# Performance work log

Measured on AMD Instinct MI355X. Metric: run time of the kernel, lower is better.

## Reference

```python
import jax, jax.numpy as jnp
import numpy as np

K = 10  # num_s nearest neighbors


def setup_inputs() -> dict:
    key = jax.random.key(0)
    k1, k2, k3, k4 = jax.random.split(key, 4)
    B, N, D, DO = 128, 50000, 384, 2048
    return {
        "targets": jax.random.normal(k1, (B, D), dtype=jnp.float32),
        "data": jax.random.normal(k2, (N, D), dtype=jnp.float32),
        "OTinput": jax.random.normal(k3, (N, D), dtype=jnp.float32),
        "OToutput": jax.random.normal(k4, (N, DO), dtype=jnp.float32),
    }


def reference(targets, data, OTinput, OToutput):
    # torch.cdist (p=2): sqrt(||t||^2 + ||d||^2 - 2 t.d), computed via one GEMM
    t2 = jnp.sum(targets * targets, axis=1, keepdims=True)        # [B, 1]
    d2 = jnp.sum(data * data, axis=1)[None, :]                    # [1, N]
    sq = t2 + d2 - 2.0 * jnp.einsum('bd,nd->bn', targets, data)  # [B, N]
    dist = jnp.sqrt(jnp.maximum(sq, 0.0))
    # topk smallest -> top_k of negated distances
    _, indices = jax.lax.top_k(-dist, K)                          # [B, K]
    input_local = OTinput[indices]                                # [B, K, D]
    output_local = OToutput[indices]                              # [B, K, DO]
    return input_local, output_local
```

## Files before the change

### kernel.cpp

```cpp
#include <hip/hip_runtime.h>

#define DIM   384
#define DIMO  2048
#define KNN   10
#define KSEL  16
#define FINF  3.0e38f
#define BK    64
#define PITCH 72

typedef __attribute__((ext_vector_type(8))) short short8v;
typedef __attribute__((ext_vector_type(4))) float float4v;

__device__ __forceinline__ unsigned short f2bf(float x) {
    union { float f; unsigned u; } c; c.f = x;
    unsigned lsb = (c.u >> 16) & 1u;
    return (unsigned short)((c.u + 0x7FFFu + lsb) >> 16);
}

__global__ __launch_bounds__(256) void score_topk_kernel(
    const float* __restrict__ tgt,
    const float* __restrict__ dat,
    float* __restrict__ cand_s,
    int*   __restrict__ cand_i,
    int N, int nblk)
{
    __shared__ unsigned short tAB[2 * 128 * PITCH];
    unsigned short* tA = tAB;
    unsigned short* tB = tAB + 128 * PITCH;
    float (*sc)[129] = reinterpret_cast<float(*)[129]>(tAB);
    __shared__ float d2p[128][8];
    __shared__ float d2s[128];

    const int tid   = threadIdx.x;
    const int nbase = blockIdx.x * 128;
    const int lane  = tid & 63;
    const int wv    = tid >> 6;
    const int wr    = wv >> 1;
    const int wc    = wv & 1;
    const int r0    = tid >> 3;
    const int c8    = tid & 7;

    const int frow  = lane & 15;
    const int kg    = lane >> 4;

    float4v acc[4][4];
#pragma unroll
    for (int i = 0; i < 4; ++i)
#pragma unroll
        for (int j = 0; j < 4; ++j) acc[i][j] = (float4v){0.f, 0.f, 0.f, 0.f};

    float d2acc[4] = {0.f, 0.f, 0.f, 0.f};

    for (int k0 = 0; k0 < DIM; k0 += BK) {
        __syncthreads();
#pragma unroll
        for (int it = 0; it < 4; ++it) {
            int row = it * 32 + r0;
            const float* s = &tgt[row * DIM + k0 + c8 * 8];
            float4 u0 = *reinterpret_cast<const float4*>(s);
            float4 u1 = *reinterpret_cast<const float4*>(s + 4);
            short8v h;
            h[0] = (short)f2bf(u0.x); h[1] = (short)f2bf(u0.y);
            h[2] = (short)f2bf(u0.z); h[3] = (short)f2bf(u0.w);
            h[4] = (short)f2bf(u1.x); h[5] = (short)f2bf(u1.y);
            h[6] = (short)f2bf(u1.z); h[7] = (short)f2bf(u1.w);
            *reinterpret_cast<short8v*>(&tA[row * PITCH + c8 * 8]) = h;
        }
#pragma unroll
        for (int it = 0; it < 4; ++it) {
            int row = it * 32 + r0;
            int g   = nbase + row;
            float4 u0 = make_float4(0.f, 0.f, 0.f, 0.f);
            float4 u1 = make_float4(0.f, 0.f, 0.f, 0.f);
            if (g < N) {
                const float* s = &dat[(size_t)g * DIM + k0 + c8 * 8];
                u0 = *reinterpret_cast<const float4*>(s);
                u1 = *reinterpret_cast<const float4*>(s + 4);
            }
            d2acc[it] += u0.x * u0.x + u0.y * u0.y + u0.z * u0.z + u0.w * u0.w
                       + u1.x * u1.x + u1.y * u1.y + u1.z * u1.z + u1.w * u1.w;
            short8v h;
            h[0] = (short)f2bf(u0.x); h[1] = (short)f2bf(u0.y);
            h[2] = (short)f2bf(u0.z); h[3] = (short)f2bf(u0.w);
            h[4] = (short)f2bf(u1.x); h[5] = (short)f2bf(u1.y);
            h[6] = (short)f2bf(u1.z); h[7] = (short)f2bf(u1.w);
            *reinterpret_cast<short8v*>(&tB[row * PITCH + c8 * 8]) = h;
        }
        __syncthreads();
#pragma unroll
        for (int ks = 0; ks < 2; ++ks) {
            short8v a[4], b[4];
            const int koff = ks * 32 + kg * 8;
#pragma unroll
            for (int f = 0; f < 4; ++f) {
                a[f] = *reinterpret_cast<const short8v*>(
                    &tA[(wr * 64 + f * 16 + frow) * PITCH + koff]);
                b[f] = *reinterpret_cast<const short8v*>(
                    &tB[(wc * 64 + f * 16 + frow) * PITCH + koff]);
            }
#pragma unroll
            for (int fr = 0; fr < 4; ++fr)
#pragma unroll
                for (int fc = 0; fc < 4; ++fc)
                    acc[fr][fc] = __builtin_amdgcn_mfma_f32_16x16x32_bf16(
                        a[fr], b[fc], acc[fr][fc], 0, 0, 0);
        }
    }

    __syncthreads();
#pragma unroll
    for (int it = 0; it < 4; ++it) d2p[it * 32 + r0][c8] = d2acc[it];
    __syncthreads();
    if (tid < 128) {
        float s = 0.f;
#pragma unroll
        for (int j = 0; j < 8; ++j) s += d2p[tid][j];
        d2s[tid] = s;
    }

    const int M = nblk * KNN;
    for (int h = 0; h < 2; ++h) {
        __syncthreads();
        if (wr == h) {
#pragma unroll
            for (int fr = 0; fr < 4; ++fr)
#pragma unroll
                for (int fc = 0; fc < 4; ++fc)
#pragma unroll
                    for (int e = 0; e < 4; ++e) {
                        int lr = fr * 16 + kg * 4 + e;
                        int lc = wc * 64 + fc * 16 + frow;
                        int n  = nbase + lc;
                        sc[lr][lc] = (n < N) ? d2s[lc] - 2.f * acc[fr][fc][e]
                                             : FINF;
                    }
        }
        __syncthreads();
        if (tid < 64) {
            int grow = h * 64 + tid;
            float ts[KNN];
            int   ti[KNN];
#pragma unroll
            for (int k = 0; k < KNN; ++k) { ts[k] = FINF; ti[k] = 0x7fffffff; }
            for (int c = 0; c < 128; ++c) {
                float s = sc[tid][c];
                if (s < ts[KNN - 1]) {
                    ts[KNN - 1] = s;
                    ti[KNN - 1] = nbase + c;
#pragma unroll
                    for (int p = KNN - 1; p > 0; --p) {
                        if (ts[p] < ts[p - 1]) {
                            float fs = ts[p]; ts[p] = ts[p - 1]; ts[p - 1] = fs;
                            int   fi = ti[p]; ti[p] = ti[p - 1]; ti[p - 1] = fi;
                        }
                    }
                }
            }
            size_t base = (size_t)grow * M + (size_t)blockIdx.x * KNN;
#pragma unroll
            for (int k = 0; k < KNN; ++k) {
                cand_s[base + k] = ts[k];
                cand_i[base + k] = ti[k];
            }
        }
    }
}

__global__ __launch_bounds__(256) void select_rescore_kernel(
    const float* __restrict__ cand_s,
    const int*   __restrict__ cand_i,
    const float* __restrict__ tgt,
    const float* __restrict__ dat,
    int* __restrict__ seldev,
    int M)
{
    const int b   = blockIdx.x;
    const int tid = threadIdx.x;
    const float* rs_ = cand_s + (size_t)b * M;
    const int*   ri_ = cand_i + (size_t)b * M;

    float ts[KSEL];
    int   ti[KSEL];
#pragma unroll
    for (int k = 0; k < KSEL; ++k) { ts[k] = FINF; ti[k] = 0x7fffffff; }

    for (int j = tid; j < M; j += 256) {
        float s  = rs_[j];
        int   id = ri_[j];
        if (s < ts[KSEL - 1] || (s == ts[KSEL - 1] && id < ti[KSEL - 1])) {
            ts[KSEL - 1] = s;
            ti[KSEL - 1] = id;
#pragma unroll
            for (int p = KSEL - 1; p > 0; --p) {
                bool sw = (ts[p] < ts[p - 1]) ||
                          (ts[p] == ts[p - 1] && ti[p] < ti[p - 1]);
                if (sw) {
                    float fs = ts[p]; ts[p] = ts[p - 1]; ts[p - 1] = fs;
                    int   fi = ti[p]; ti[p] = ti[p - 1]; ti[p - 1] = fi;
                }
            }
        }
    }

    __shared__ float cs[256 * KSEL];
    __shared__ int   ci[256 * KSEL];
    __shared__ float rs[256];
    __shared__ int   ri[256];
    __shared__ int   rt[256];
    __shared__ int   sel16[KSEL];
    __shared__ float ex_s[KSEL];
    __shared__ int   ex_i[KSEL];

#pragma unroll
    for (int k = 0; k < KSEL; ++k) {
        cs[tid * KSEL + k] = ts[k];
        ci[tid * KSEL + k] = ti[k];
    }

    int ptr = 0;
    for (int k = 0; k < KSEL; ++k) {
        rs[tid] = cs[tid * KSEL + ptr];
        ri[tid] = ci[tid * KSEL + ptr];
        rt[tid] = tid;
        __syncthreads();
        for (int off = 128; off > 0; off >>= 1) {
            if (tid < off) {
                float s2 = rs[tid + off]; int i2 = ri[tid + off];
                float s1 = rs[tid];       int i1 = ri[tid];
                if (s2 < s1 || (s2 == s1 && i2 < i1)) {
                    rs[tid] = s2; ri[tid] = i2; rt[tid] = rt[tid + off];
                }
            }
            __syncthreads();
        }
        if (tid == 0) sel16[k] = ri[0];
        if (tid == rt[0]) ptr++;
        __syncthreads();
    }

    if (tid < KSEL) {
        const int n = sel16[tid];
        float d2p_[8] = {0.f, 0.f, 0.f, 0.f, 0.f, 0.f, 0.f, 0.f};
        float dot = 0.f;
        for (int c = 0; c < DIM / 32; ++c) {
#pragma unroll
            for (int j = 0; j < 8; ++j) {
                const float4 v = *reinterpret_cast<const float4*>(
                    &dat[(size_t)n * DIM + c * 32 + j * 4]);
                const float4 t = *reinterpret_cast<const float4*>(
                    &tgt[(size_t)b * DIM + c * 32 + j * 4]);
                d2p_[j] += v.x * v.x + v.y * v.y + v.z * v.z + v.w * v.w;
                dot = fmaf(t.x, v.x, dot);
                dot = fmaf(t.y, v.y, dot);
                dot = fmaf(t.z, v.z, dot);
                dot = fmaf(t.w, v.w, dot);
            }
        }
        float d2 = 0.f;
#pragma unroll
        for (int j = 0; j < 8; ++j) d2 += d2p_[j];
        ex_s[tid] = d2 - 2.f * dot;
        ex_i[tid] = n;
    }
    __syncthreads();

    if (tid == 0) {
        float fs[KNN]; int fi[KNN];
#pragma unroll
        for (int k = 0; k < KNN; ++k) { fs[k] = FINF; fi[k] = 0x7fffffff; }
        for (int q = 0; q < KSEL; ++q) {
            float s  = ex_s[q];
            int   id = ex_i[q];
            if (s < fs[KNN - 1] || (s == fs[KNN - 1] && id < fi[KNN - 1])) {
                fs[KNN - 1] = s;
                fi[KNN - 1] = id;
#pragma unroll
                for (int p = KNN - 1; p > 0; --p) {
                    bool sw = (fs[p] < fs[p - 1]) ||
                              (fs[p] == fs[p - 1] && fi[p] < fi[p - 1]);
                    if (sw) {
                        float a = fs[p]; fs[p] = fs[p - 1]; fs[p - 1] = a;
                        int   i2 = fi[p]; fi[p] = fi[p - 1]; fi[p - 1] = i2;
                    }
                }
            }
        }
#pragma unroll
        for (int k = 0; k < KNN; ++k) seldev[b * KNN + k] = fi[k];
    }
}

__global__ __launch_bounds__(256) void gather_kernel(
    const int* __restrict__ seldev,
    const float* __restrict__ OTin,
    const float* __restrict__ OTout,
    float* __restrict__ out,
    int B)
{
    const int bid = blockIdx.x;
    const int tid = threadIdx.x;
    const int idx = seldev[bid];
    const size_t o1 = (size_t)B * KNN * DIM;

    const float4* in4  = reinterpret_cast<const float4*>(&OTin[(size_t)idx * DIM]);
    float4*       out4 = reinterpret_cast<float4*>(&out[(size_t)bid * DIM]);
    for (int q = tid; q < DIM / 4; q += 256) out4[q] = in4[q];

    const float4* ino4  = reinterpret_cast<const float4*>(&OTout[(size_t)idx * DIMO]);
    float4*       outo4 = reinterpret_cast<float4*>(&out[o1 + (size_t)bid * DIMO]);
    for (int q = tid; q < DIMO / 4; q += 256) outo4[q] = ino4[q];
}

extern "C" void kernel_launch(void* const* d_in, const int* in_sizes, int n_in,
                              void* d_out, int out_size, void* d_ws, size_t ws_size,
                              hipStream_t stream) {
    const float* targets = (const float*)d_in[0];
    const float* data    = (const float*)d_in[1];
    const float* OTin    = (const float*)d_in[2];
    const float* OTout   = (const float*)d_in[3];
    float* out = (float*)d_out;

    const int B = in_sizes[0] / DIM;
    const int N = in_sizes[1] / DIM;

    const int nblk = (N + 127) / 128;
    const int M    = nblk * KNN;

    float* cand_s = (float*)d_ws;
    int*   cand_i = (int*)(cand_s + (size_t)B * M);
    int*   seldev = (int*)(cand_i + (size_t)B * M);

    score_topk_kernel<<<nblk, 256, 0, stream>>>(targets, data, cand_s, cand_i, N, nblk);
    select_rescore_kernel<<<B, 256, 0, stream>>>(cand_s, cand_i, targets, data, seldev, M);
    gather_kernel<<<B * KNN, 256, 0, stream>>>(seldev, OTin, OTout, out, B);
}
```

Baseline: 147.2 us.

## Fuse gather into select kernel and replace shared-memory merge with wave shuffles

Merges the gather kernel into the select/rescore kernel so each batch row's block copies its 10 selected OTinput/OToutput rows directly, removing a launch and the seldev round trip. The 16-round shared-memory tree reduction with many __syncthreads is replaced by per-wave shuffle-based argmin merges followed by a single-wave merge of the four wave winners. The bf16 conversion helper now uses the HIP intrinsic. The gather now runs on only B=128 blocks instead of 1280, which may reduce memory-level parallelism for the copy.

```diff
diff --git a/kernel.cpp b/kernel.cpp
--- a/kernel.cpp
+++ b/kernel.cpp
@@ -1,4 +1,5 @@
 #include <hip/hip_runtime.h>
+#include <hip/hip_bf16.h>
 
 #define DIM   384
 #define DIMO  2048
@@ -12,9 +13,7 @@
 typedef __attribute__((ext_vector_type(4))) float float4v;
 
 __device__ __forceinline__ unsigned short f2bf(float x) {
-    union { float f; unsigned u; } c; c.f = x;
-    unsigned lsb = (c.u >> 16) & 1u;
-    return (unsigned short)((c.u + 0x7FFFu + lsb) >> 16);
+    return __bfloat16_as_ushort(__float2bfloat16(x));
 }
 
 __global__ __launch_bounds__(256) void score_topk_kernel(
@@ -166,16 +165,20 @@
     }
 }
 
-__global__ __launch_bounds__(256) void select_rescore_kernel(
+__global__ __launch_bounds__(256) void select_rescore_gather_kernel(
     const float* __restrict__ cand_s,
     const int*   __restrict__ cand_i,
     const float* __restrict__ tgt,
     const float* __restrict__ dat,
-    int* __restrict__ seldev,
-    int M)
+    const float* __restrict__ OTin,
+    const float* __restrict__ OTout,
+    float* __restrict__ out,
+    int M, int B)
 {
-    const int b   = blockIdx.x;
-    const int tid = threadIdx.x;
+    const int b    = blockIdx.x;
+    const int tid  = threadIdx.x;
+    const int lane = tid & 63;
+    const int wv   = tid >> 6;
     const float* rs_ = cand_s + (size_t)b * M;
     const int*   ri_ = cand_i + (size_t)b * M;
 
@@ -202,41 +205,66 @@
         }
     }
 
-    __shared__ float cs[256 * KSEL];
-    __shared__ int   ci[256 * KSEL];
-    __shared__ float rs[256];
-    __shared__ int   ri[256];
-    __shared__ int   rt[256];
+    __shared__ float ls[256 * KSEL];
+    __shared__ int   li[256 * KSEL];
+    __shared__ float wout_s[4 * KSEL];
+    __shared__ int   wout_i[4 * KSEL];
     __shared__ int   sel16[KSEL];
     __shared__ float ex_s[KSEL];
     __shared__ int   ex_i[KSEL];
+    __shared__ int   selk[KNN];
 
 #pragma unroll
     for (int k = 0; k < KSEL; ++k) {
-        cs[tid * KSEL + k] = ts[k];
-        ci[tid * KSEL + k] = ti[k];
-    }
-
-    int ptr = 0;
-    for (int k = 0; k < KSEL; ++k) {
-        rs[tid] = cs[tid * KSEL + ptr];
-        ri[tid] = ci[tid * KSEL + ptr];
-        rt[tid] = tid;
-        __syncthreads();
-        for (int off = 128; off > 0; off >>= 1) {
-            if (tid < off) {
-                float s2 = rs[tid + off]; int i2 = ri[tid + off];
-                float s1 = rs[tid];       int i1 = ri[tid];
-                if (s2 < s1 || (s2 == s1 && i2 < i1)) {
-                    rs[tid] = s2; ri[tid] = i2; rt[tid] = rt[tid + off];
+        ls[tid * KSEL + k] = ts[k];
+        li[tid * KSEL + k] = ti[k];
+    }
+
+    {
+        int   hp = 0;
+        float hs = ts[0];
+        int   hi = ti[0];
+#pragma unroll
+        for (int k = 0; k < KSEL; ++k) {
+            float ms = hs; int mi = hi;
+#pragma unroll
+            for (int m = 32; m > 0; m >>= 1) {
+                float s2 = __shfl_xor(ms, m);
+                int   i2 = __shfl_xor(mi, m);
+                if (s2 < ms || (s2 == ms && i2 < mi)) { ms = s2; mi = i2; }
+            }
+            if (lane == 0) { wout_s[wv * KSEL + k] = ms; wout_i[wv * KSEL + k] = mi; }
+            bool iwin = (hs == ms) && (hi == mi);
+            if (iwin) {
+                if (hp < KSEL - 1) {
+                    ++hp;
+                    hs = ls[tid * KSEL + hp];
+                    hi = li[tid * KSEL + hp];
+                } else {
+                    hs = FINF; hi = 0x7fffffff;
                 }
             }
-            __syncthreads();
-        }
-        if (tid == 0) sel16[k] = ri[0];
-        if (tid == rt[0]) ptr++;
-        __syncthreads();
-    }
+        }
+    }
+    __syncthreads();
+
+    if (wv == 0) {
+        float s = wout_s[lane];
+        int   i = wout_i[lane];
+#pragma unroll
+        for (int k = 0; k < KSEL; ++k) {
+            float ms = s; int mi = i;
+#pragma unroll
+            for (int m = 32; m > 0; m >>= 1) {
+                float s2 = __shfl_xor(ms, m);
+                int   i2 = __shfl_xor(mi, m);
+                if (s2 < ms || (s2 == ms && i2 < mi)) { ms = s2; mi = i2; }
+            }
+            if (lane == 0) sel16[k] = mi;
+            if (s == ms && i == mi) { s = FINF; i = 0x7fffffff; }
+        }
+    }
+    __syncthreads();
 
     if (tid < KSEL) {
         const int n = sel16[tid];
@@ -286,29 +314,30 @@
             }
         }
 #pragma unroll
-        for (int k = 0; k < KNN; ++k) seldev[b * KNN + k] = fi[k];
-    }
-}
-
-__global__ __launch_bounds__(256) void gather_kernel(
-    const int* __restrict__ seldev,
-    const float* __restrict__ OTin,
-    const float* __restrict__ OTout,
-    float* __restrict__ out,
-    int B)
-{
-    const int bid = blockIdx.x;
-    const int tid = threadIdx.x;
-    const int idx = seldev[bid];
+        for (int k = 0; k < KNN; ++k) selk[k] = fi[k];
+    }
+    __syncthreads();
+
     const size_t o1 = (size_t)B * KNN * DIM;
-
-    const float4* in4  = reinterpret_cast<const float4*>(&OTin[(size_t)idx * DIM]);
-    float4*       out4 = reinterpret_cast<float4*>(&out[(size_t)bid * DIM]);
-    for (int q = tid; q < DIM / 4; q += 256) out4[q] = in4[q];
-
-    const float4* ino4  = reinterpret_cast<const float4*>(&OTout[(size_t)idx * DIMO]);
-    float4*       outo4 = reinterpret_cast<float4*>(&out[o1 + (size_t)bid * DIMO]);
-    for (int q = tid; q < DIMO / 4; q += 256) outo4[q] = ino4[q];
+    const float4* in4  = reinterpret_cast<const float4*>(OTin);
+    const float4* ino4 = reinterpret_cast<const float4*>(OTout);
+    float4* out4  = reinterpret_cast<float4*>(out);
+    float4* outo4 = reinterpret_cast<float4*>(out + o1);
+
+    for (int q = tid; q < KNN * (DIM / 4); q += 256) {
+        int k = q / (DIM / 4);
+        int c = q - k * (DIM / 4);
+        int idx = selk[k];
+        out4[((size_t)b * KNN + k) * (DIM / 4) + c] =
+            in4[(size_t)idx * (DIM / 4) + c];
+    }
+    for (int q = tid; q < KNN * (DIMO / 4); q += 256) {
+        int k = q / (DIMO / 4);
+        int c = q - k * (DIMO / 4);
+        int idx = selk[k];
+        outo4[((size_t)b * KNN + k) * (DIMO / 4) + c] =
+            ino4[(size_t)idx * (DIMO / 4) + c];
+    }
 }
 
 extern "C" void kernel_launch(void* const* d_in, const int* in_sizes, int n_in,
@@ -328,9 +357,8 @@
 
     float* cand_s = (float*)d_ws;
     int*   cand_i = (int*)(cand_s + (size_t)B * M);
-    int*   seldev = (int*)(cand_i + (size_t)B * M);
 
     score_topk_kernel<<<nblk, 256, 0, stream>>>(targets, data, cand_s, cand_i, N, nblk);
-    select_rescore_kernel<<<B, 256, 0, stream>>>(cand_s, cand_i, targets, data, seldev, M);
-    gather_kernel<<<B * KNN, 256, 0, stream>>>(seldev, OTin, OTout, out, B);
+    select_rescore_gather_kernel<<<B, 256, 0, stream>>>(
+        cand_s, cand_i, targets, data, OTin, OTout, out, M, B);
 }
```

New measurement: 156.8 us. +6.6%, slower.
